# Optimization experiments

Measured on AMD Instinct MI355X. Metric: run time of the kernel, lower is better.

Reference implementation:

```python
import jax, jax.numpy as jnp
import numpy as np

SIGMA_LOW = 0.2
SIGMA_HIGH = 0.01
DT = 0.1


def _gauss_kernel(sigma):
    # tw always uses sigma_low for its range, as in the original __init__
    tw = jnp.arange(-3.0 * SIGMA_LOW, 3.0 * SIGMA_LOW, 0.001 * DT, dtype=jnp.float32)  # 12000 taps
    g = jnp.exp(-0.5 * (tw / sigma) ** 2)
    return g / jnp.sum(g)


def _same_corr_fft(x, w):
    """tf.nn.conv1d(x, w_shared, stride=1, padding='SAME') where the same 1-D
    kernel w is applied to every channel independently (shared-weight depthwise).
    x: (1, T, C) NWC, w: (K,). FFT-based since K=12000 taps."""
    T = x.shape[1]
    K = w.shape[0]
    N = T + K - 1                      # full linear correlation length
    pad_left = (K - 1) // 2            # TF SAME left padding
    Xf = jnp.fft.rfft(x, n=N, axis=1)
    Wf = jnp.fft.rfft(w[::-1], n=N)    # flip kernel: correlation via convolution
    z = jnp.fft.irfft(Xf * Wf[None, :, None], n=N, axis=1)  # (1, N, C)
    start = K - 1 - pad_left           # offset of SAME output inside full result
    return jax.lax.dynamic_slice_in_dim(z, start, T, axis=1)


def setup_inputs() -> dict:
    key = jax.random.key(0)
    firings = jax.random.normal(key, (1, 100000, 512), dtype=jnp.float32)
    sel_idx = jnp.arange(256, dtype=jnp.int32)  # static boolean mask -> gather indices
    return {
        "firings": firings,
        "gauss_low": _gauss_kernel(SIGMA_LOW),
        "gauss_high": _gauss_kernel(SIGMA_HIGH),
        "sel_idx": sel_idx,
    }


def reference(firings, gauss_low, gauss_high, sel_idx):
    # boolean_mask(firings, mask, axis=2) -> channel gather
    sel = jnp.take(firings, sel_idx, axis=2)              # (1, T, Csel)
    low = _same_corr_fft(sel, gauss_low)                  # low-pass component
    filt = sel - low + jnp.mean(low)                      # high-pass + restore global mean
    return _same_corr_fft(filt, gauss_high)               # smooth with narrow Gaussian
```

## Files before the change

kernel.cpp:

```cpp
#include <hip/hip_runtime.h>
#include <hip/hip_bf16.h>

#define T_LEN   100000
#define C_SEL   256
#define C_IN    512
#define KLOW    12000
#define B1      50
#define NB1     2000
#define ND1     2001
#define NW1     241
#define ND2E    5003
#define WH_OFF  5500
#define KH      1001
#define MLEN    5000
#define TR      50
#define NBLK    2000
#define NAC     53
#define NSLOT   21

typedef __attribute__((ext_vector_type(4))) float f32x4;

__device__ __forceinline__ void stage16(const float* g, float* l){
  __builtin_amdgcn_global_load_lds((const __attribute__((address_space(1))) void*)g,
                                   (__attribute__((address_space(3))) void*)l,
                                   16, 0, 0);
}

__global__ __launch_bounds__(256) void kA_prep(const float* __restrict__ wlow,
                                               const float* __restrict__ whigh,
                                               float* __restrict__ W1,
                                               float* __restrict__ musum,
                                               float* __restrict__ cwh,
                                               float* __restrict__ wht){
  if (blockIdx.x == 0){
    int m1 = threadIdx.x;
    if (m1 == 0) musum[0] = 0.f;
    if (m1 < NW1){
      float s = 0.f;
      int kbase = 50*m1 - 1;
      for (int off = 0; off < 50; ++off){
        int k = kbase + off;
        if (k >= 0 && k < KLOW) s += wlow[k];
      }
      W1[m1] = s * (1.0f/50.0f);
    }
    for (int k = threadIdx.x; k < 20*51; k += 256){
      int pp = k / 51, u = k - 51*pp;
      int j = 20*u + pp - 1;
      wht[k] = (j >= 0 && j < KH) ? whigh[WH_OFF + j] : 0.f;
    }
  } else {
    __shared__ float part[256];
    __shared__ float pre[257];
    int tg = threadIdx.x;
    float s = 0.f;
    #pragma unroll
    for (int r = 0; r < 4; ++r){ int j = 4*tg + r; if (j < KH) s += whigh[WH_OFF + j]; }
    part[tg] = s;
    __syncthreads();
    if (tg == 0){
      float run = 0.f; pre[0] = 0.f;
      for (int k = 0; k < 256; ++k){ run += part[k]; pre[k+1] = run; }
      cwh[0] = 0.f;
    }
    __syncthreads();
    float base = pre[tg], r0 = 0.f;
    #pragma unroll
    for (int r = 0; r < 4; ++r){
      int j = 4*tg + r;
      if (j < KH){ r0 += whigh[WH_OFF + j]; cwh[j+1] = base + r0; }
    }
  }
}

template<int PAR>
__device__ __forceinline__ void tile_conv(const float (*tile)[C_SEL],
                                          const float* __restrict__ whtl,
                                          int tid, float* acc, float& ssum){
  #pragma unroll 1
  for (int pp = 0; pp < 10; ++pp){
    f32x4 tpc[13];
    #pragma unroll
    for (int c = 0; c < 13; ++c)
      tpc[c] = *reinterpret_cast<const f32x4*>(&whtl[pp*52 + 4*c]);
    if (PAR == 0){
      float v0 = tile[pp][tid], v1 = tile[20+pp][tid], v2 = tile[40+pp][tid];
      ssum += v0 + v1 + v2;
      #pragma unroll
      for (int u = 0; u < 51; ++u){
        float tp = tpc[u>>2][u&3];
        acc[50-u] += tp*v0; acc[51-u] += tp*v1; acc[52-u] += tp*v2;
      }
    } else {
      float v1 = tile[10+pp][tid], v2 = tile[30+pp][tid];
      ssum += v1 + v2;
      #pragma unroll
      for (int u = 0; u < 51; ++u){
        float tp = tpc[u>>2][u&3];
        acc[51-u] += tp*v1; acc[52-u] += tp*v2;
      }
    }
  }
  #pragma unroll 1
  for (int pp = 10; pp < 20; ++pp){
    f32x4 tpc[13];
    #pragma unroll
    for (int c = 0; c < 13; ++c)
      tpc[c] = *reinterpret_cast<const f32x4*>(&whtl[pp*52 + 4*c]);
    if (PAR == 0){
      float v0 = tile[pp][tid], v1 = tile[20+pp][tid];
      ssum += v0 + v1;
      #pragma unroll
      for (int u = 0; u < 51; ++u){
        float tp = tpc[u>>2][u&3];
        acc[50-u] += tp*v0; acc[51-u] += tp*v1;
      }
    } else {
      float v0 = tile[pp-10][tid], v1 = tile[pp+10][tid], v2 = tile[pp+30][tid];
      ssum += v0 + v1 + v2;
      #pragma unroll
      for (int u = 0; u < 51; ++u){
        float tp = tpc[u>>2][u&3];
        acc[50-u] += tp*v0; acc[51-u] += tp*v1; acc[52-u] += tp*v2;
      }
    }
  }
}

template<int PAR>
__device__ __forceinline__ void tile_store(const float* acc, int mbase, int b,
                                           int tid, float* __restrict__ pbuf){
  float* pb = pbuf + (size_t)(b % NSLOT)*C_SEL + tid;
  #pragma unroll
  for (int a = (PAR ? 1 : 0); a < NAC; ++a){
    int jo = mbase - 24 + a;
    if (jo >= 0 && jo < ND2E) pb[(size_t)jo*(NSLOT*C_SEL)] = acc[a];
  }
}

__global__ __launch_bounds__(256) void kC_conv(const float* __restrict__ x,
                                               const int* __restrict__ sel,
                                               const float* __restrict__ wht,
                                               float* __restrict__ S,
                                               float* __restrict__ pbuf){
  __shared__ float tile[TR][C_SEL];
  __shared__ float whtl[20*52];
  __shared__ int okf;
  int tid = threadIdx.x;
  int b   = blockIdx.x;
  int lane = tid & 63, wid = tid >> 6;
  if (tid == 0) okf = 1;
  __syncthreads();
  if (sel[tid] != tid) okf = 0;
  for (int k = tid; k < 20*52; k += 256){
    int pp = k / 52, u = k - 52*pp;
    whtl[k] = (u < 51) ? wht[pp*51 + u] : 0.f;
  }
  __syncthreads();
  const float* xrow0 = x + (size_t)b*(TR*C_IN);
  if (okf){
    for (int i = wid; i < TR; i += 4)
      stage16(xrow0 + (size_t)i*C_IN + 4*lane, &tile[i][0]);
    asm volatile("s_waitcnt vmcnt(0)" ::: "memory");
    __syncthreads();
  } else {
    int sc = sel[tid];
    for (int i = 0; i < TR; ++i) tile[i][tid] = xrow0[(size_t)i*C_IN + sc];
    __syncthreads();
  }
  float acc[NAC];
  #pragma unroll
  for (int a = 0; a < NAC; ++a) acc[a] = 0.f;
  float ssum = 0.f;
  int mbase = (b >> 1)*5 + (b & 1)*2;
  if (b & 1){ tile_conv<1>(tile, whtl, tid, acc, ssum); tile_store<1>(acc, mbase, b, tid, pbuf); }
  else      { tile_conv<0>(tile, whtl, tid, acc, ssum); tile_store<0>(acc, mbase, b, tid, pbuf); }
  S[b*C_SEL + tid] = ssum;
}

__global__ __launch_bounds__(256) void kB_lowd(const float* __restrict__ S,
                                               const float* __restrict__ W1,
                                               float* __restrict__ lowd,
                                               float* __restrict__ musum){
  __shared__ float w1s[NW1];
  int tid = threadIdx.x;
  if (tid < NW1) w1s[tid] = W1[tid];
  __syncthreads();
  int jd   = blockIdx.x*4 + (tid >> 6);
  int lane = tid & 63;
  if (jd >= ND1) return;
  int lo = 120 - jd;  if (lo < 0)   lo = 0;
  int hi = 2119 - jd; if (hi > 240) hi = 240;
  f32x4 acc = {0.f, 0.f, 0.f, 0.f};
  #pragma unroll 4
  for (int m1 = lo; m1 <= hi; ++m1){
    int jb = jd + m1 - 120;
    acc += w1s[m1] * *reinterpret_cast<const f32x4*>(S + (size_t)jb*C_SEL + 4*lane);
  }
  *reinterpret_cast<f32x4*>(lowd + (size_t)jd*C_SEL + 4*lane) = acc;
  float t = acc.x + acc.y + acc.z + acc.w;
  for (int off = 32; off > 0; off >>= 1) t += __shfl_down(t, off);
  if (lane == 0){
    float ew = (jd == 0) ? 25.5f : ((jd == ND1-1) ? 24.5f : 50.f);
    atomicAdd(musum, ew*t);
  }
}

__global__ __launch_bounds__(256) void kC_red(const float* __restrict__ pbuf,
                                              const float* __restrict__ cwh,
                                              const float* __restrict__ lowd,
                                              const float* __restrict__ musum,
                                              float* __restrict__ outd){
  int tid = threadIdx.x;
  int jo  = blockIdx.x*4 + (tid >> 6);
  int j   = tid & 63;
  if (jo >= ND2E) return;
  int tlo = 20*jo - 519; if (tlo < 0) tlo = 0;
  int thi = 20*jo + 481; if (thi > T_LEN-1) thi = T_LEN-1;
  int blo = tlo/TR, bhi = thi/TR;
  int cnt = bhi - blo + 1;
  int sb  = blo % NSLOT;
  const float* base = pbuf + (size_t)jo*(NSLOT*C_SEL) + 4*j;
  f32x4 a = {0.f, 0.f, 0.f, 0.f};
  #pragma unroll
  for (int k = 0; k < NSLOT; ++k){
    f32x4 v = *reinterpret_cast<const f32x4*>(base + (size_t)k*C_SEL);
    int d = k - sb; if (d < 0) d += NSLOT;
    bool ok = (d < cnt);
    a.x += ok ? v.x : 0.f;
    a.y += ok ? v.y : 0.f;
    a.z += ok ? v.z : 0.f;
    a.w += ok ? v.w : 0.f;
  }
  float mu = musum[0] * (1.0f/((float)T_LEN*(float)C_SEL));
  int tn = 20*(jo - 1);
  int jmin = 499 - tn;             if (jmin < 0) jmin = 0;
  int jmax = T_LEN - 1 + 499 - tn; if (jmax > 1000) jmax = 1000;
  float s = cwh[jmax + 1] - cwh[jmin];
  int tc = tn < 0 ? 0 : (tn > T_LEN-1 ? T_LEN-1 : tn);
  int jd = tc/50, rr = tc - 50*jd;
  float fr = rr*(1.f/50.f);
  f32x4 l0 = *reinterpret_cast<const f32x4*>(lowd + (size_t)jd*C_SEL + 4*j);
  f32x4 l1 = *reinterpret_cast<const f32x4*>(lowd + (size_t)(jd+1)*C_SEL + 4*j);
  f32x4 lo = l0 + (l1 - l0)*fr;
  *reinterpret_cast<f32x4*>(outd + (size_t)jo*C_SEL + 4*j) = a + (mu - lo)*s;
}

__global__ __launch_bounds__(256) void kD_interp(const float* __restrict__ outd,
                                                 float* __restrict__ out){
  int tid  = threadIdx.x;
  int lane = tid & 63;
  int w    = tid >> 6;
  int t0   = blockIdx.x*8;
  #pragma unroll
  for (int k = 0; k < 2; ++k){
    int t = t0 + w + 4*k;
    int jo = t/20, rr = t - jo*20;
    float a = rr*(1.f/20.f);
    const float* bb = outd + (size_t)jo*C_SEL + 4*lane;
    f32x4 p0 = *reinterpret_cast<const f32x4*>(bb);
    f32x4 p1 = *reinterpret_cast<const f32x4*>(bb +   C_SEL);
    f32x4 p2 = *reinterpret_cast<const f32x4*>(bb + 2*C_SEL);
    f32x4 p3 = *reinterpret_cast<const f32x4*>(bb + 3*C_SEL);
    f32x4 m = p1 + 0.5f*a*((p2 - p0)
            + a*((2.f*p0 - 5.f*p1 + 4.f*p2 - p3)
            + a*(3.f*(p1 - p2) + p3 - p0)));
    *reinterpret_cast<f32x4*>(out + (size_t)t*C_SEL + 4*lane) = m;
  }
}

extern "C" void kernel_launch(void* const* d_in, const int* in_sizes, int n_in,
                              void* d_out, int out_size, void* d_ws, size_t ws_size,
                              hipStream_t stream){
  const float* firings = (const float*)d_in[0];
  const float* glow    = (const float*)d_in[1];
  const float* ghigh   = (const float*)d_in[2];
  const int*   sel     = (const int*)d_in[3];
  float* out = (float*)d_out;
  float* ws  = (float*)d_ws;

  float* W1    = ws;
  float* musum = ws + 256;
  float* cwh   = ws + 320;
  float* wht   = ws + 1344;
  float* S     = ws + 2560;
  float* lowd  = ws + 514560;
  float* outd  = ws + 1026816;
  float* pbuf  = ws + 2307584;

  hipLaunchKernelGGL(kA_prep,  dim3(2),        dim3(256), 0, stream,
                     glow, ghigh, W1, musum, cwh, wht);
  hipLaunchKernelGGL(kC_conv,  dim3(NBLK),     dim3(256), 0, stream,
                     firings, sel, wht, S, pbuf);
  hipLaunchKernelGGL(kB_lowd,  dim3(501),      dim3(256), 0, stream, S, W1, lowd, musum);
  hipLaunchKernelGGL(kC_red,   dim3(1251),     dim3(256), 0, stream,
                     pbuf, cwh, lowd, musum, outd);
  hipLaunchKernelGGL(kD_interp,dim3(T_LEN/8),  dim3(256), 0, stream, outd, out);
}
```

Measured before the change: 396.7 us.

## Process four 50-row tiles per block and accumulate overlapping partials in registers

Each conv block now loops over four consecutive 50-row tiles and adds their partial correlation outputs into one shared 60-entry register accumulator, instead of each 50-row tile writing 53 partial outputs to a 21-slot buffer. This cuts the partial-sum traffic to global memory and shrinks the number of slots the downstream reduction must sum. In exchange there are four times fewer blocks (500) and more registers per thread, which may reduce occupancy and latency hiding. Loads for each tile are serialized with syncs rather than overlapped.

```diff
diff --git a/kernel.cpp b/kernel.cpp
--- a/kernel.cpp
+++ b/kernel.cpp
@@ -12,11 +12,10 @@
 #define ND2E    5003
 #define WH_OFF  5500
 #define KH      1001
-#define MLEN    5000
-#define TR      50
-#define NBLK    2000
-#define NAC     53
-#define NSLOT   21
+#define TR      200
+#define NBLK    500
+#define NAC     60
+#define NSLOT   6
 
 typedef __attribute__((ext_vector_type(4))) float f32x4;
 
@@ -127,23 +126,12 @@
   }
 }
 
-template<int PAR>
-__device__ __forceinline__ void tile_store(const float* acc, int mbase, int b,
-                                           int tid, float* __restrict__ pbuf){
-  float* pb = pbuf + (size_t)(b % NSLOT)*C_SEL + tid;
-  #pragma unroll
-  for (int a = (PAR ? 1 : 0); a < NAC; ++a){
-    int jo = mbase - 24 + a;
-    if (jo >= 0 && jo < ND2E) pb[(size_t)jo*(NSLOT*C_SEL)] = acc[a];
-  }
-}
-
 __global__ __launch_bounds__(256) void kC_conv(const float* __restrict__ x,
                                                const int* __restrict__ sel,
                                                const float* __restrict__ wht,
                                                float* __restrict__ S,
                                                float* __restrict__ pbuf){
-  __shared__ float tile[TR][C_SEL];
+  __shared__ float tile[50][C_SEL];
   __shared__ float whtl[20*52];
   __shared__ int okf;
   int tid = threadIdx.x;
@@ -157,25 +145,37 @@
     whtl[k] = (u < 51) ? wht[pp*51 + u] : 0.f;
   }
   __syncthreads();
-  const float* xrow0 = x + (size_t)b*(TR*C_IN);
-  if (okf){
-    for (int i = wid; i < TR; i += 4)
-      stage16(xrow0 + (size_t)i*C_IN + 4*lane, &tile[i][0]);
-    asm volatile("s_waitcnt vmcnt(0)" ::: "memory");
+  float acc[NAC];
+  #pragma unroll
+  for (int a = 0; a < NAC; ++a) acc[a] = 0.f;
+  int ok = okf;
+  int sc = sel[tid];
+  #pragma unroll
+  for (int q = 0; q < 4; ++q){
+    const float* xrow0 = x + (size_t)(4*b + q)*(50*C_IN);
+    if (ok){
+      for (int i = wid; i < 50; i += 4)
+        stage16(xrow0 + (size_t)i*C_IN + 4*lane, &tile[i][0]);
+      asm volatile("s_waitcnt vmcnt(0)" ::: "memory");
+      __syncthreads();
+    } else {
+      for (int i = 0; i < 50; ++i) tile[i][tid] = xrow0[(size_t)i*C_IN + sc];
+      __syncthreads();
+    }
+    float ssum = 0.f;
+    const int off = 5*(q>>1) + 2*(q&1);
+    if (q & 1) tile_conv<1>(tile, whtl, tid, acc + off, ssum);
+    else       tile_conv<0>(tile, whtl, tid, acc + off, ssum);
+    S[(4*b + q)*C_SEL + tid] = ssum;
     __syncthreads();
-  } else {
-    int sc = sel[tid];
-    for (int i = 0; i < TR; ++i) tile[i][tid] = xrow0[(size_t)i*C_IN + sc];
-    __syncthreads();
-  }
-  float acc[NAC];
-  #pragma unroll
-  for (int a = 0; a < NAC; ++a) acc[a] = 0.f;
-  float ssum = 0.f;
-  int mbase = (b >> 1)*5 + (b & 1)*2;
-  if (b & 1){ tile_conv<1>(tile, whtl, tid, acc, ssum); tile_store<1>(acc, mbase, b, tid, pbuf); }
-  else      { tile_conv<0>(tile, whtl, tid, acc, ssum); tile_store<0>(acc, mbase, b, tid, pbuf); }
-  S[b*C_SEL + tid] = ssum;
+  }
+  float* pb = pbuf + (size_t)(b % NSLOT)*C_SEL + tid;
+  int jo0 = 10*b - 24;
+  #pragma unroll
+  for (int a = 0; a < NAC; ++a){
+    int jo = jo0 + a;
+    if (jo >= 0 && jo < ND2E) pb[(size_t)jo*(NSLOT*C_SEL)] = acc[a];
+  }
 }
 
 __global__ __launch_bounds__(256) void kB_lowd(const float* __restrict__ S,
```

Result: faster. 380.7 us (-4.0%).
